# Performance work log

Measured on AMD Instinct MI355X. Metric: run time of the kernel, lower is better.

## Reference

```python
import jax, jax.numpy as jnp
import numpy as np

# ---- constants corresponding to undefined globals in the source repo ----
LN2 = float(np.log(2.0))
SIGMA2 = 1.0
W_F_COM, W_F_CRB = 1.0, 0.5
W_W_COM, W_W_CRB = 1.0, 0.5
BETA, EPS, ETA_F, ETA_W = 0.9, 1e-8, 0.01, 0.01


def _H(x):
    return jnp.conj(jnp.swapaxes(x, -1, -2))


def project_unit_modulus(F, eps=1e-12):
    mag = jnp.abs(F)
    safe = jnp.where(mag > eps, mag, 1.0).astype(F.dtype)
    return jnp.where(mag > eps, F / safe, jnp.zeros((), F.dtype))


def _power(F, W):
    # trace(F W W^H F^H) per (A,B) batch element, real
    FW = F @ W
    return jnp.sum(jnp.abs(FW) ** 2, axis=(-2, -1))


def normalize_power(F, W, Pt):
    s = jnp.sqrt(Pt / _power(F, W))
    return F * s[..., None, None].astype(F.dtype)


def normalize(F, W, Pt):
    s = jnp.sqrt(Pt / _power(F, W))
    return F, W * s[..., None, None].astype(W.dtype)


def grad_F_com(H, F, W):
    # H:[A,B,M,N]  F:[A,B,N,R]  W:[A,B,R,M]
    K_d = W.shape[0]
    V = W @ _H(W)                                   # [A,B,R,R]
    w_cols = jnp.swapaxes(W, -1, -2)[..., None]     # [A,B,M,R,1]
    V_mk = V[:, :, None] - w_cols @ _H(w_cols)      # [A,B,M,R,R]
    h = H[..., None]                                # [A,B,M,N,1]
    hHF = _H(h) @ F[:, :, None]                     # [A,B,M,1,R] = h^H F
    qf1 = (hHF @ V[:, :, None] @ _H(hHF))[..., 0, 0]   # h^H F V F^H h
    qf2 = (hHF @ V_mk @ _H(hHF))[..., 0, 0]
    d1 = LN2 * (qf1 + SIGMA2) + 1e-4
    d2 = LN2 * (qf2 + SIGMA2) + 1e-4
    HtF = h @ hHF                                   # [A,B,M,N,R] = (h h^H) F
    g1 = (HtF @ V[:, :, None]) / d1[..., None, None]
    g2 = (HtF @ V_mk) / d2[..., None, None]
    return (g1 - g2).sum(axis=2) / K_d


def _crb_core(F, W, A_dot, R_N_inv):
    Mm = _H(A_dot) @ R_N_inv @ A_dot                # [N,N]
    FHMF = _H(F) @ Mm @ F                           # [A,B,R,R]
    inner = _H(W) @ FHMF @ W                        # [A,B,M,M]
    tr = jnp.trace(inner, axis1=-2, axis2=-1)       # [A,B]
    return Mm, FHMF, tr


def grad_F_crb(F, W, A_dot, R_N_inv):
    Mm, _, tr = _crb_core(F, W, A_dot, R_N_inv)
    num = Mm @ F @ (W @ _H(W))                      # [A,B,N,R]
    return num / tr.reshape(1, -1, 1, 1)


def grad_W_crb(F, W, A_dot, R_N_inv):
    _, FHMF, tr = _crb_core(F, W, A_dot, R_N_inv)
    return (FHMF @ W) / tr.reshape(1, -1, 1, 1)


def grad_W_com(H, F, W):
    # Vectorised form of the per-antenna/user loop. In the original,
    # grad_W_1 == grad_W_2, so grad1 - masked(grad2) keeps only column m of term m.
    Mu = W.shape[-1]
    V = W @ _H(W)
    FHh = _H(F)[:, :, None] @ H[..., None]          # [A,B,M,R,1]
    Hbar = FHh @ _H(FHh)                            # [A,B,M,R,R] = F^H h h^H F
    tr = jnp.einsum('abij,abmji->abm', V, Hbar)     # trace(W W^H Hbar_m)
    denom = LN2 * (tr + SIGMA2)
    G = (Hbar @ W[:, :, None]) / denom[..., None, None]   # [A,B,M,R,M]
    return jnp.einsum('abmim->abim', G) / Mu


def get_sum_rate(H, F, W):
    G = jnp.abs(jnp.conj(H) @ F @ W) ** 2           # [A,B,M,M], (m,k)=|h_m^H F w_k|^2
    sig = jnp.diagonal(G, axis1=-2, axis2=-1)
    interf = G.sum(-1) - sig
    return jnp.log2(1.0 + sig / (interf + SIGMA2)).sum(-1)[0]   # [B]


def get_crb_fe(F, W, xi_0, A_dot, R_N_inv):
    _, _, tr = _crb_core(F, W, A_dot, R_N_inv)
    return (1.0 / (2.0 * xi_0 ** 2 * jnp.real(tr) + 1e-12))[0]  # [B]


def run_pga(H, F, W, xi_0, A_dot, R_N_inv, Pt, n_outer, n_inner, track=True):
    F = project_unit_modulus(F)
    F, W = normalize(F, W, Pt)
    B = H.shape[1]
    rates = jnp.zeros((n_outer, n_inner + 1, B), jnp.float32)
    crbs = jnp.zeros((n_outer, n_inner + 1, B), jnp.float32)
    s_F = jnp.zeros_like(F)
    s_W = jnp.zeros_like(W)
    for ii in range(n_outer):
        for jj in range(n_inner):
            gF = grad_F_com(H, F, W) * W_F_COM + grad_F_crb(F, W, A_dot, R_N_inv) * W_F_CRB
            s_F = BETA * s_F + (1.0 - BETA) * gF
            F = F + ETA_F * gF / (jnp.sqrt(s_F) + EPS)
            F = normalize_power(F, W, Pt)
            if track:
                rates = rates.at[ii, jj + 1].set(jax.lax.stop_gradient(get_sum_rate(H, F, W)))
                crbs = crbs.at[ii, jj + 1].set(jax.lax.stop_gradient(get_crb_fe(F, W, xi_0, A_dot, R_N_inv)))
        F = project_unit_modulus(F)
        gW0 = grad_W_com(H, F, W)[0] * W_W_COM + grad_W_crb(F, W, A_dot, R_N_inv)[0] * W_W_CRB
        s_W = s_W.at[0].set(BETA * s_W[0] + (1.0 - BETA) * gW0)
        W = W.at[0].set(W[0] + ETA_W * gW0 / (jnp.sqrt(s_W[0]) + EPS))
        F, W = normalize(F, W, Pt)
        if track:
            rates = rates.at[ii, 0].set(jax.lax.stop_gradient(get_sum_rate(H, F, W)))
            crbs = crbs.at[ii, 0].set(jax.lax.stop_gradient(get_crb_fe(F, W, xi_0, A_dot, R_N_inv)))
    rates = rates.reshape(n_outer * (n_inner + 1), B).T
    crbs = crbs.reshape(n_outer * (n_inner + 1), B).T
    return rates, crbs, F, W


def setup_inputs() -> dict:
    key = jax.random.key(0)
    ks = jax.random.split(key, 12)
    A, B, Mu, N, R, L = 1, 1024, 8, 64, 16, 64
    f32 = jnp.float32
    inp = dict(
        H_re=jax.random.normal(ks[0], (A, B, Mu, N), f32),
        H_im=jax.random.normal(ks[1], (A, B, Mu, N), f32),
        F0_re=jax.random.normal(ks[2], (A, B, N, R), f32),
        F0_im=jax.random.normal(ks[3], (A, B, N, R), f32),
        W0_re=jax.random.normal(ks[4], (A, B, R, Mu), f32),
        W0_im=jax.random.normal(ks[5], (A, B, R, Mu), f32),
        A_dot_re=jax.random.normal(ks[6], (L, N), f32),
        A_dot_im=jax.random.normal(ks[7], (L, N), f32),
    )
    # Build a PSD noise-covariance inverse so CRB trace denominators are well-conditioned.
    C = (jax.random.normal(ks[8], (L, L), f32) + 1j * jax.random.normal(ks[9], (L, L), f32)).astype(jnp.complex64)
    Rinv = (C @ jnp.conj(C.T)) / L + jnp.eye(L, dtype=jnp.complex64)
    inp['R_N_inv_re'] = jnp.real(Rinv)
    inp['R_N_inv_im'] = jnp.imag(Rinv)
    inp['xi_0'] = jnp.ones((1,), f32)
    inp['Pt'] = 10
    inp['n_iter_outer'] = 5
    inp['n_iter_inner'] = 4
    return inp


def reference(H_re, H_im, F0_re, F0_im, W0_re, W0_im, A_dot_re, A_dot_im,
              R_N_inv_re, R_N_inv_im, xi_0, Pt, n_iter_outer, n_iter_inner):
    c64 = jnp.complex64
    H = (H_re + 1j * H_im).astype(c64)
    F = (F0_re + 1j * F0_im).astype(c64)
    W = (W0_re + 1j * W0_im).astype(c64)
    A_dot = (A_dot_re + 1j * A_dot_im).astype(c64)
    R_N_inv = (R_N_inv_re + 1j * R_N_inv_im).astype(c64)
    return run_pga(H, F, W, xi_0, A_dot, R_N_inv, float(Pt), int(n_iter_outer), int(n_iter_inner), track=True)
```

## Files before the change

### kernel.cpp

```cpp
#include <hip/hip_runtime.h>
#include <math.h>

typedef float2 cf;

__device__ __forceinline__ cf mkc(float x, float y){ return make_float2(x,y); }
__device__ __forceinline__ cf lo4(float4 v){ return mkc(v.x, v.y); }
__device__ __forceinline__ cf hi4(float4 v){ return mkc(v.z, v.w); }


__device__ __forceinline__ void cmad(cf& acc, cf a, cf b){
    asm("v_pk_fma_f32 %0, %1, %2, %0 op_sel:[1,1,0] op_sel_hi:[1,0,1] neg_lo:[0,1,0]\n\t"
        "v_pk_fma_f32 %0, %1, %2, %0 op_sel:[0,0,0] op_sel_hi:[0,1,1]"
        : "+v"(acc) : "v"(a), "v"(b));
}
__device__ __forceinline__ void cmadc(cf& acc, cf a, cf b){
    asm("v_pk_fma_f32 %0, %1, %2, %0 op_sel:[1,1,0] op_sel_hi:[1,0,1] neg_hi:[0,1,0]\n\t"
        "v_pk_fma_f32 %0, %1, %2, %0 op_sel:[0,0,0] op_sel_hi:[0,1,1]"
        : "+v"(acc) : "v"(a), "v"(b));
}
__device__ __forceinline__ void cmad_bc(cf& acc, cf a, cf b){
    asm("v_pk_fma_f32 %0, %1, %2, %0 op_sel:[1,1,0] op_sel_hi:[0,1,1] neg_hi:[0,1,0]\n\t"
        "v_pk_fma_f32 %0, %1, %2, %0 op_sel:[0,0,0] op_sel_hi:[1,0,1]"
        : "+v"(acc) : "v"(a), "v"(b));
}
__device__ __forceinline__ void cmad_cc(cf& acc, cf a, cf b){
    asm("v_pk_fma_f32 %0, %1, %2, %0 op_sel:[1,1,0] op_sel_hi:[1,0,1] neg_lo:[0,1,0] neg_hi:[0,1,0]\n\t"
        "v_pk_fma_f32 %0, %1, %2, %0 op_sel:[0,0,0] op_sel_hi:[0,1,1] neg_hi:[0,1,0]"
        : "+v"(acc) : "v"(a), "v"(b));
}
__device__ __forceinline__ cf csqrtf2(cf z){
    float x = z.x, y = z.y;
    float r = hypotf(x, y);
    if (r == 0.0f) return mkc(0.f, 0.f);
    if (x >= 0.0f){
        float t = sqrtf(0.5f*(r + x));
        return mkc(t, 0.5f*y/t);
    } else {
        float t = sqrtf(0.5f*(r - x));
        return mkc(0.5f*fabsf(y)/t, copysignf(t, y));
    }
}
__device__ __forceinline__ cf cdiv(cf a, cf b){
    float inv = 1.0f/(b.x*b.x + b.y*b.y);
    return mkc((a.x*b.x + a.y*b.y)*inv, (a.y*b.x - a.x*b.y)*inv);
}

#define LN2F  0.69314718055994530942f
#define BETA_ 0.9f
#define OMB_  0.1f
#define EPS_  1e-8f
#define ETAF_ 0.01f
#define ETAW_ 0.01f

#define MM_S 66
#define F_S  18
#define FT_S 66
#define H_S  66
#define U_S  18
#define V_S  18

__device__ cf g_Mm[4096];

__device__ __forceinline__ float readScalarF(const int* p){
    int iv = *p;
    if (iv >= 0 && iv < 1000000) return (float)iv;
    return __int_as_float(iv);
}
__device__ __forceinline__ int readScalarI(const int* p){
    int iv = *p;
    if (iv >= 0 && iv < 1000000) return iv;
    return (int)(__int_as_float(iv) + 0.5f);
}

__device__ __forceinline__ float blockReduceSum(float v, float* slot, int tid){
    #pragma unroll
    for (int o = 32; o > 0; o >>= 1) v += __shfl_down(v, o, 64);
    if ((tid & 63) == 0) slot[tid >> 6] = v;
    __syncthreads();
    return slot[0] + slot[1] + slot[2] + slot[3];
}
__device__ __forceinline__ float2 blockReduceSum2(float a, float b2, float* sA, float* sB, int tid){
    #pragma unroll
    for (int o = 32; o > 0; o >>= 1){ a += __shfl_down(a, o, 64); b2 += __shfl_down(b2, o, 64); }
    if ((tid & 63) == 0){ sA[tid >> 6] = a; sB[tid >> 6] = b2; }
    __syncthreads();
    return make_float2(sA[0]+sA[1]+sA[2]+sA[3], sB[0]+sB[1]+sB[2]+sB[3]);
}

__device__ __forceinline__ void computeMF_T(const cf* sMm, const cf* sFT, cf* sMF, int tid){
    int j = tid & 15, nb = tid >> 4;
    cf a0=mkc(0,0), a1=mkc(0,0), a2=mkc(0,0), a3=mkc(0,0);
    const float4* ftrow = (const float4*)(sFT + j*FT_S);
    #pragma unroll
    for (int kkb = 0; kkb < 4; kkb++){
        cf f[16];
        #pragma unroll
        for (int q = 0; q < 8; q++){
            float4 v = ftrow[kkb*8+q];
            f[2*q] = lo4(v); f[2*q+1] = hi4(v);
        }
        const float4* m0 = (const float4*)(sMm + (nb    )*MM_S + kkb*16);
        const float4* m1 = (const float4*)(sMm + (nb+16 )*MM_S + kkb*16);
        const float4* m2 = (const float4*)(sMm + (nb+32 )*MM_S + kkb*16);
        const float4* m3 = (const float4*)(sMm + (nb+48 )*MM_S + kkb*16);
        #pragma unroll
        for (int q = 0; q < 8; q++){
            float4 v0 = m0[q], v1 = m1[q], v2 = m2[q], v3 = m3[q];
            cmad(a0, lo4(v0), f[2*q]); cmad(a0, hi4(v0), f[2*q+1]);
            cmad(a1, lo4(v1), f[2*q]); cmad(a1, hi4(v1), f[2*q+1]);
            cmad(a2, lo4(v2), f[2*q]); cmad(a2, hi4(v2), f[2*q+1]);
            cmad(a3, lo4(v3), f[2*q]); cmad(a3, hi4(v3), f[2*q+1]);
        }
    }
    sMF[(nb   )*F_S+j]=a0; sMF[(nb+16)*F_S+j]=a1;
    sMF[(nb+32)*F_S+j]=a2; sMF[(nb+48)*F_S+j]=a3;
}

__device__ __forceinline__ void uRefresh(const cf* sH, const cf* sFT, cf* sU, int tid){
    int h = tid & 1, j = (tid >> 1) & 15, m = tid >> 5;
    const float4* hp = (const float4*)(sH  + m*H_S);
    const float4* fp = (const float4*)(sFT + j*FT_S);
    cf acc = mkc(0,0);
    #pragma unroll
    for (int q = 0; q < 16; q++){
        int c = 2*q + h;
        float4 hv = hp[c], fv = fp[c];
        cmadc(acc, lo4(hv), lo4(fv));
        cmadc(acc, hi4(hv), hi4(fv));
    }
    acc.x += __shfl_xor(acc.x, 1, 64);
    acc.y += __shfl_xor(acc.y, 1, 64);
    if (h == 0) sU[m*U_S+j] = acc;
}

__device__ __forceinline__ float fwPartialOnly(const cf* sF, const cf* sW, int tid){
    int k = tid & 7, nb = tid >> 3;
    cf wcol[16];
    #pragma unroll
    for (int r = 0; r < 16; r++) wcol[r] = sW[r*8+k];
    float part = 0.f;
    #pragma unroll
    for (int rep = 0; rep < 2; rep++){
        int n = nb + rep*32;
        const float4* fr = (const float4*)(sF + n*F_S);
        cf acc = mkc(0,0);
        #pragma unroll
        for (int q = 0; q < 8; q++){
            float4 v = fr[q];
            cmad(acc, lo4(v), wcol[2*q]); cmad(acc, hi4(v), wcol[2*q+1]);
        }
        part += acc.x*acc.x + acc.y*acc.y;
    }
    return part;
}

__device__ __forceinline__ float2 fwTrcPartial(const cf* sF, const cf* sMF, const cf* sW, int tid){
    int k = tid & 7, nb = tid >> 3;
    cf wcol[16];
    #pragma unroll
    for (int r = 0; r < 16; r++) wcol[r] = sW[r*8+k];
    float part = 0.f, ptrc = 0.f;
    #pragma unroll
    for (int rep = 0; rep < 2; rep++){
        int n = nb + rep*32;
        const float4* fr = (const float4*)(sF + n*F_S);
        const float4* mr = (const float4*)(sMF + n*F_S);
        cf acc = mkc(0,0), acm = mkc(0,0);
        #pragma unroll
        for (int q = 0; q < 8; q++){
            float4 v = fr[q], m = mr[q];
            cmad(acc, lo4(v), wcol[2*q]); cmad(acc, hi4(v), wcol[2*q+1]);
            cmad(acm, lo4(m), wcol[2*q]); cmad(acm, hi4(m), wcol[2*q+1]);
        }
        part += acc.x*acc.x + acc.y*acc.y;
        ptrc += acc.x*acm.x + acc.y*acm.y;
    }
    return make_float2(part, ptrc);
}

__device__ __forceinline__ void ratesWave3(const cf* sU, const cf* sW, float mul,
                                           float* sRateVal, int tid){
    if (tid < 192) return;
    int l = tid - 192, m = l >> 3, k = l & 7;
    cf acc = mkc(0,0);
    #pragma unroll
    for (int j = 0; j < 16; j++) cmad(acc, sU[m*U_S+j], sW[j*8+k]);
    float p = acc.x*acc.x + acc.y*acc.y;
    float tot = p;
    #pragma unroll
    for (int mask = 4; mask >= 1; mask >>= 1) tot += __shfl_xor(tot, mask, 8);
    float sig = __shfl(p, 9*m, 64);
    float rate = log2f(1.0f + (mul*sig)/fmaf(mul, tot - sig, 1.0f));
    float val = (k == 0) ? rate : 0.0f;
    #pragma unroll
    for (int mask = 32; mask >= 1; mask >>= 1) val += __shfl_xor(val, mask, 64);
    if (l == 0) *sRateVal = val;
}

__global__ __launch_bounds__(256) void pga_prep(
    const float* __restrict__ Ar, const float* __restrict__ Ai,
    const float* __restrict__ Rr, const float* __restrict__ Ri)
{
    __shared__ cf sA[4096];
    __shared__ cf Tc[512];
    int tid = threadIdx.x;
    for (int idx = tid; idx < 4096; idx += 256)
        sA[idx] = mkc(Ar[idx], Ai[idx]);
    __syncthreads();
    for (int jb = 0; jb < 8; jb++){
        int j0 = jb*8;
        #pragma unroll
        for (int rep = 0; rep < 2; rep++){
            int idx = tid + rep*256;
            int p = idx >> 3, jc = idx & 7;
            cf acc = mkc(0,0);
            for (int q = 0; q < 64; q++){
                cf rv = mkc(Rr[p*64+q], Ri[p*64+q]);
                cmad(acc, rv, sA[q*64 + j0 + jc]);
            }
            Tc[idx] = acc;
        }
        __syncthreads();
        #pragma unroll
        for (int rep = 0; rep < 2; rep++){
            int idx = tid + rep*256;
            int i = idx >> 3, jc = idx & 7;
            cf acc = mkc(0,0);
            for (int p = 0; p < 64; p++)
                cmadc(acc, sA[p*64+i], Tc[p*8+jc]);
            g_Mm[i*64 + j0 + jc] = acc;
        }
        __syncthreads();
    }
}

__global__ __launch_bounds__(256) void pga_main(
    const float* __restrict__ Hre, const float* __restrict__ Him,
    const float* __restrict__ F0re, const float* __restrict__ F0im,
    const float* __restrict__ W0re, const float* __restrict__ W0im,
    const float* __restrict__ xi0p,
    const int* __restrict__ Ptp, const int* __restrict__ noutp, const int* __restrict__ ninnp,
    float* __restrict__ out, int B, int cplx)
{
    const int tid = threadIdx.x;
    const int b = blockIdx.x;

    __shared__ __align__(16) char sPool[72640];
    __shared__ float sRed[12];
    __shared__ float sRateVal;

    cf* sMm   = (cf*)(sPool + 0);
    cf* sF    = (cf*)(sPool + 33792);
    cf* sMF   = (cf*)(sPool + 43008);
    cf* sFT   = (cf*)(sPool + 52224);
    cf* sH    = (cf*)(sPool + 60672);
    cf* sW    = (cf*)(sPool + 64896);
    cf* sV    = (cf*)(sPool + 65920);
    cf* sU    = (cf*)(sPool + 68224);
    cf* sRow  = (cf*)(sPool + 69376);
    cf* sFHMF = (cf*)(sPool + 70400);
    cf* sCoefC= (cf*)(sPool + 72576);

    const float Pt    = readScalarF(Ptp);
    const int n_outer = readScalarI(noutp);
    const int n_inner = readScalarI(ninnp);
    const float xi0   = xi0p[0];
    const int nt = n_outer * (n_inner + 1);
    const float cxi = 2.0f*xi0*xi0;

    float* outR = out;
    float* outC = out + (size_t)B * nt;
    float* outF = out + (size_t)2 * B * nt;
    float* outW = outF + (cplx ? (size_t)B * 2048 : (size_t)B * 1024);

    cf fsf[4]; cf ssw = mkc(0.f, 0.f);
    {
        for (int idx = tid; idx < 4096; idx += 256){
            int r = idx >> 6, c = idx & 63;
            sMm[r*MM_S+c] = g_Mm[idx];
        }
        const float* hr = Hre + (size_t)b*512;
        const float* hi = Him + (size_t)b*512;
        for (int idx = tid; idx < 512; idx += 256){
            int m = idx >> 6, n = idx & 63;
            sH[m*H_S+n] = mkc(hr[idx], hi[idx]);
        }
        const float* fr = F0re + (size_t)b*1024;
        const float* fi = F0im + (size_t)b*1024;
        for (int idx = tid; idx < 1024; idx += 256){
            int n = idx >> 4, r = idx & 15;
            float re = fr[idx], im = fi[idx];
            float mag = hypotf(re, im);
            cf f = (mag > 1e-12f) ? mkc(re/mag, im/mag) : mkc(0.f, 0.f);
            sF[n*F_S+r] = f;
            sFT[r*FT_S+n] = f;
        }
        if (tid < 128)
            sW[tid] = mkc(W0re[(size_t)b*128 + tid], W0im[(size_t)b*128 + tid]);
        #pragma unroll
        for (int rep = 0; rep < 4; rep++) fsf[rep] = mkc(0.f, 0.f);
    }
    __syncthreads();

    uRefresh(sH, sFT, sU, tid);
    {
        float pw0 = blockReduceSum(fwPartialOnly(sF, sW, tid), sRed+0, tid);
        float s0 = sqrtf(Pt / pw0);
        if (tid < 128){ cf w = sW[tid]; sW[tid] = mkc(w.x*s0, w.y*s0); }
    }
    computeMF_T(sMm, sFT, sMF, tid);
    __syncthreads();

    float sp = 1.0f, sp2 = 1.0f;

    for (int ii = 0; ii < n_outer; ii++){
        {
            int i = tid >> 4, jx = tid & 15;
            cf acc = mkc(0,0);
            #pragma unroll
            for (int k = 0; k < 8; k++) cmad_bc(acc, sW[i*8+k], sW[jx*8+k]);
            sV[i*V_S+jx] = acc;
        }
        __syncthreads();

        for (int jj = 0; jj < n_inner; jj++){
            const int j = tid & 15, nb = tid >> 4;

            cf vrow[16];
            {
                const float4* vp = (const float4*)(sV + j*V_S);
                #pragma unroll
                for (int q = 0; q < 8; q++){
                    float4 v = vp[q];
                    vrow[2*q] = lo4(v); vrow[2*q+1] = hi4(v);
                }
            }
            float ptr_ = 0.f;
            cf G[4];
            #pragma unroll
            for (int rep = 0; rep < 4; rep++){
                int n = nb + rep*16;
                const float4* mr = (const float4*)(sMF + n*F_S);
                cf acc = mkc(0,0);
                #pragma unroll
                for (int q = 0; q < 8; q++){
                    float4 v = mr[q];
                    cmad_bc(acc, lo4(v), vrow[2*q]); cmad_bc(acc, hi4(v), vrow[2*q+1]);
                }
                G[rep] = acc;
                cf f = sF[n*F_S+j];
                ptr_ += f.x*acc.x + f.y*acc.y;
            }
            if (tid < 128){
                int m = tid >> 4;
                const float4* up = (const float4*)(sU + m*U_S);
                cf t2 = mkc(0,0);
                #pragma unroll
                for (int q = 0; q < 8; q++){
                    float4 uv = up[q];
                    cmad_bc(t2, lo4(uv), vrow[2*q]); cmad_bc(t2, hi4(uv), vrow[2*q+1]);
                }
                cf u = sU[m*U_S+j];
                float qv = t2.x*u.x + t2.y*u.y;
                cf c = mkc(0,0); cmad(c, u, sW[j*8+m]);
                #pragma unroll
                for (int mask = 8; mask >= 1; mask >>= 1){
                    qv  += __shfl_xor(qv,  mask, 16);
                    c.x += __shfl_xor(c.x, mask, 16);
                    c.y += __shfl_xor(c.y, mask, 16);
                }
                float cc = c.x*c.x + c.y*c.y;
                float inv1 = 1.0f/(LN2F*(sp2*qv + 1.0f) + 1e-4f);
                float inv2 = 1.0f/(LN2F*(sp2*(qv - cc) + 1.0f) + 1e-4f);
                float a = inv1 - inv2;
                cf ci = mkc(c.x*inv2, c.y*inv2);
                cf row = mkc(t2.x*a, t2.y*a);
                cmad_bc(row, ci, sW[j*8+m]);
                sRow[tid] = row;
            }
            if (jj > 0) ratesWave3(sU, sW, sp2, &sRateVal, tid);
            float tr = blockReduceSum(ptr_, sRed+0, tid);
            if (jj > 0 && tid == 0){
                int t = ii*(n_inner+1) + jj;
                size_t base = (size_t)b*nt;
                outR[base + t] = sRateVal;
                outC[base + t] = 1.0f/(cxi*(sp2*tr) + 1e-12f);
            }

            {
                float hinv = 0.5f/(sp*tr);
                cf rowj[8];
                #pragma unroll
                for (int m = 0; m < 8; m++){
                    cf r = sRow[m*16+j];
                    rowj[m] = mkc(sp*r.x, sp*r.y);
                }
                #pragma unroll
                for (int rep = 0; rep < 4; rep++){
                    int n = nb + rep*16;
                    cf g = mkc(G[rep].x*hinv, G[rep].y*hinv);
                    #pragma unroll
                    for (int m = 0; m < 8; m++) cmad(g, sH[m*H_S+n], rowj[m]);
                    cf sf = fsf[rep];
                    sf.x = BETA_*sf.x + OMB_*g.x;
                    sf.y = BETA_*sf.y + OMB_*g.y;
                    fsf[rep] = sf;
                    cf d = csqrtf2(sf); d.x += EPS_;
                    cf upd = cdiv(g, d);
                    cf f = sF[n*F_S+j];
                    cf fn = mkc(fmaf(ETAF_, upd.x, sp*f.x), fmaf(ETAF_, upd.y, sp*f.y));
                    sF[n*F_S+j] = fn;
                    sFT[j*FT_S+n] = fn;
                }
            }
            __syncthreads();

            computeMF_T(sMm, sFT, sMF, tid);
            float part = fwPartialOnly(sF, sW, tid);
            uRefresh(sH, sFT, sU, tid);
            float pw = blockReduceSum(part, sRed+4, tid);
            float s = sqrtf(Pt / pw);
            sp = s; sp2 = s*s;

            if (jj == n_inner-1){
                cf vrow2[16];
                {
                    const float4* vp2 = (const float4*)(sV + j*V_S);
                    #pragma unroll
                    for (int q = 0; q < 8; q++){
                        float4 v = vp2[q];
                        vrow2[2*q] = lo4(v); vrow2[2*q+1] = hi4(v);
                    }
                }
                float ptrl = 0.f;
                #pragma unroll
                for (int rep = 0; rep < 4; rep++){
                    int n = nb + rep*16;
                    const float4* mr = (const float4*)(sMF + n*F_S);
                    cf acc = mkc(0,0);
                    #pragma unroll
                    for (int q = 0; q < 8; q++){
                        float4 v = mr[q];
                        cmad_bc(acc, lo4(v), vrow2[2*q]); cmad_bc(acc, hi4(v), vrow2[2*q+1]);
                    }
                    cf f = sF[n*F_S+j];
                    ptrl += f.x*acc.x + f.y*acc.y;
                }
                ratesWave3(sU, sW, sp2, &sRateVal, tid);
                float trl = blockReduceSum(ptrl, sRed+8, tid);
                if (tid == 0){
                    int t = ii*(n_inner+1) + n_inner;
                    size_t base = (size_t)b*nt;
                    outR[base + t] = sRateVal;
                    outC[base + t] = 1.0f/(cxi*(sp2*trl) + 1e-12f);
                }
            }
        }

        const int j = tid & 15, nb = tid >> 4;
        {
            #pragma unroll
            for (int rep = 0; rep < 4; rep++){
                int n = nb + rep*16;
                cf f = sF[n*F_S+j];
                float mag = hypotf(f.x, f.y);
                cf fp = (sp*mag > 1e-12f) ? mkc(f.x/mag, f.y/mag) : mkc(0.f, 0.f);
                sF[n*F_S+j] = fp;
                sFT[j*FT_S+n] = fp;
            }
            sp = 1.0f; sp2 = 1.0f;
        }
        __syncthreads();
        computeMF_T(sMm, sFT, sMF, tid);
        uRefresh(sH, sFT, sU, tid);
        __syncthreads();
        float ptr2;
        {
            int i = tid >> 4;
            const float4* fti = (const float4*)(sFT + i*FT_S);
            cf acc = mkc(0,0);
            #pragma unroll
            for (int q = 0; q < 32; q++){
                float4 fv = fti[q];
                cmadc(acc, lo4(fv), sMF[(2*q  )*F_S+j]);
                cmadc(acc, hi4(fv), sMF[(2*q+1)*F_S+j]);
            }
            sFHMF[i*17+j] = acc;
            cf v = sV[j*V_S+i];
            ptr2 = acc.x*v.x - acc.y*v.y;
        }
        if (tid < 128){
            int m = tid >> 4, r = tid & 15;
            cf u_mr = sU[m*U_S+r];
            const float4* up = (const float4*)(sU + m*U_S);
            cf t2 = mkc(0,0);
            #pragma unroll
            for (int q = 0; q < 8; q++){
                float4 uv = up[q];
                cmad_cc(t2, sV[(2*q)*V_S+r],   lo4(uv));
                cmad_cc(t2, sV[(2*q+1)*V_S+r], hi4(uv));
            }
            float trm = u_mr.x*t2.x - u_mr.y*t2.y;
            cf a = mkc(0,0); cmad(a, u_mr, sW[r*8+m]);
            #pragma unroll
            for (int mask = 8; mask >= 1; mask >>= 1){
                trm += __shfl_xor(trm, mask, 16);
                a.x += __shfl_xor(a.x, mask, 16);
                a.y += __shfl_xor(a.y, mask, 16);
            }
            if (r == 0){
                float invd = 1.0f/(LN2F*(trm + 1.0f)*8.0f);
                sCoefC[m] = mkc(a.x*invd, a.y*invd);
            }
        }
        float trW = blockReduceSum(ptr2, sRed+0, tid);
        cf gw = mkc(0,0);
        if (tid < 128){
            int i2 = tid >> 3, mm = tid & 7;
            cf acc = mkc(0,0);
            #pragma unroll
            for (int j2 = 0; j2 < 16; j2++) cmad(acc, sFHMF[i2*17+j2], sW[j2*8+mm]);
            float hinv = 0.5f / trW;
            gw = mkc(acc.x*hinv, acc.y*hinv);
            cmadc(gw, sU[mm*U_S+i2], sCoefC[mm]);
        }
        __syncthreads();
        if (tid < 128){
            cf sw = ssw;
            sw.x = BETA_*sw.x + OMB_*gw.x;
            sw.y = BETA_*sw.y + OMB_*gw.y;
            ssw = sw;
            cf d = csqrtf2(sw); d.x += EPS_;
            cf upd = cdiv(gw, d);
            cf w = sW[tid];
            w.x = fmaf(ETAW_, upd.x, w.x);
            w.y = fmaf(ETAW_, upd.y, w.y);
            sW[tid] = w;
        }
        __syncthreads();
        float2 pq = fwTrcPartial(sF, sMF, sW, tid);
        float2 pr = blockReduceSum2(pq.x, pq.y, sRed+4, sRed+8, tid);
        float s2 = sqrtf(Pt / pr.x);
        float s2sq = s2*s2;
        ratesWave3(sU, sW, s2sq, &sRateVal, tid);
        __syncthreads();
        if (tid < 128){
            cf w = sW[tid];
            sW[tid] = mkc(w.x*s2, w.y*s2);
        }
        if (tid == 0){
            int t = ii*(n_inner+1);
            size_t base = (size_t)b*nt;
            outR[base + t] = sRateVal;
            outC[base + t] = 1.0f/(cxi*(s2sq*pr.y) + 1e-12f);
        }
        __syncthreads();
    }

    if (cplx){
        int j = tid & 15, nb = tid >> 4;
        #pragma unroll
        for (int rep = 0; rep < 4; rep++){
            int n = nb + rep*16;
            cf f = sF[n*F_S+j];
            size_t o = ((size_t)b*1024 + (size_t)(tid + rep*256))*2;
            outF[o]   = f.x;
            outF[o+1] = f.y;
        }
        if (tid < 128){
            cf w = sW[tid];
            size_t o = ((size_t)b*128 + tid)*2;
            outW[o]   = w.x;
            outW[o+1] = w.y;
        }
    } else {
        int j = tid & 15, nb = tid >> 4;
        #pragma unroll
        for (int rep = 0; rep < 4; rep++){
            int n = nb + rep*16;
            outF[(size_t)b*1024 + (size_t)(tid + rep*256)] = sF[n*F_S+j].x;
        }
        if (tid < 128)
            outW[(size_t)b*128 + tid] = sW[tid].x;
    }
}

extern "C" void kernel_launch(void* const* d_in, const int* in_sizes, int n_in,
                              void* d_out, int out_size, void* d_ws, size_t ws_size,
                              hipStream_t stream)
{
    (void)n_in; (void)d_ws; (void)ws_size;
    int B = in_sizes[0] / 512;

    long S = (long)out_size;
    long numI = S - 2304L*B;
    long numR = S - 1152L*B;
    bool okI = (numI > 0) && (numI % (2L*B) == 0) && (numI/(2L*B) >= 1) && (numI/(2L*B) <= 256);
    bool okR = (numR > 0) && (numR % (2L*B) == 0) && (numR/(2L*B) >= 1) && (numR/(2L*B) <= 256);
    int cplx = okI ? 1 : (okR ? 0 : 1);

    pga_prep<<<1, 256, 0, stream>>>(
        (const float*)d_in[6], (const float*)d_in[7],
        (const float*)d_in[8], (const float*)d_in[9]);

    pga_main<<<B, 256, 0, stream>>>(
        (const float*)d_in[0], (const float*)d_in[1],
        (const float*)d_in[2], (const float*)d_in[3],
        (const float*)d_in[4], (const float*)d_in[5],
        (const float*)d_in[10],
        (const int*)d_in[11], (const int*)d_in[12], (const int*)d_in[13],
        (float*)d_out, B, cplx);
}
```

Baseline: 663.0 us.

## Double block size to 512 threads and halve per-thread work in PGA main kernel

Launches pga_main with 512 threads per block instead of 256 and redistributes per-thread loops (MF product, power partials, gradient rows, output stores) so each thread handles half as many rows. Phases that only map to 256 threads are gated with tid<256, the rate computation moves to the last wave, and block reductions now sum eight wave slots. The aim is more latency hiding and shorter serial chains per block, at the cost of higher LDS-limited occupancy pressure, idle lanes in the gated phases, and more expensive barriers.

```diff
diff --git a/kernel.cpp b/kernel.cpp
--- a/kernel.cpp
+++ b/kernel.cpp
@@ -77,19 +77,21 @@
     for (int o = 32; o > 0; o >>= 1) v += __shfl_down(v, o, 64);
     if ((tid & 63) == 0) slot[tid >> 6] = v;
     __syncthreads();
-    return slot[0] + slot[1] + slot[2] + slot[3];
+    return ((slot[0]+slot[1])+(slot[2]+slot[3]))+((slot[4]+slot[5])+(slot[6]+slot[7]));
 }
 __device__ __forceinline__ float2 blockReduceSum2(float a, float b2, float* sA, float* sB, int tid){
     #pragma unroll
     for (int o = 32; o > 0; o >>= 1){ a += __shfl_down(a, o, 64); b2 += __shfl_down(b2, o, 64); }
     if ((tid & 63) == 0){ sA[tid >> 6] = a; sB[tid >> 6] = b2; }
     __syncthreads();
-    return make_float2(sA[0]+sA[1]+sA[2]+sA[3], sB[0]+sB[1]+sB[2]+sB[3]);
+    float ra = ((sA[0]+sA[1])+(sA[2]+sA[3]))+((sA[4]+sA[5])+(sA[6]+sA[7]));
+    float rb = ((sB[0]+sB[1])+(sB[2]+sB[3]))+((sB[4]+sB[5])+(sB[6]+sB[7]));
+    return make_float2(ra, rb);
 }
 
 __device__ __forceinline__ void computeMF_T(const cf* sMm, const cf* sFT, cf* sMF, int tid){
     int j = tid & 15, nb = tid >> 4;
-    cf a0=mkc(0,0), a1=mkc(0,0), a2=mkc(0,0), a3=mkc(0,0);
+    cf a0=mkc(0,0), a1=mkc(0,0);
     const float4* ftrow = (const float4*)(sFT + j*FT_S);
     #pragma unroll
     for (int kkb = 0; kkb < 4; kkb++){
@@ -100,20 +102,15 @@
             f[2*q] = lo4(v); f[2*q+1] = hi4(v);
         }
         const float4* m0 = (const float4*)(sMm + (nb    )*MM_S + kkb*16);
-        const float4* m1 = (const float4*)(sMm + (nb+16 )*MM_S + kkb*16);
-        const float4* m2 = (const float4*)(sMm + (nb+32 )*MM_S + kkb*16);
-        const float4* m3 = (const float4*)(sMm + (nb+48 )*MM_S + kkb*16);
+        const float4* m1 = (const float4*)(sMm + (nb+32 )*MM_S + kkb*16);
         #pragma unroll
         for (int q = 0; q < 8; q++){
-            float4 v0 = m0[q], v1 = m1[q], v2 = m2[q], v3 = m3[q];
+            float4 v0 = m0[q], v1 = m1[q];
             cmad(a0, lo4(v0), f[2*q]); cmad(a0, hi4(v0), f[2*q+1]);
             cmad(a1, lo4(v1), f[2*q]); cmad(a1, hi4(v1), f[2*q+1]);
-            cmad(a2, lo4(v2), f[2*q]); cmad(a2, hi4(v2), f[2*q+1]);
-            cmad(a3, lo4(v3), f[2*q]); cmad(a3, hi4(v3), f[2*q+1]);
-        }
-    }
-    sMF[(nb   )*F_S+j]=a0; sMF[(nb+16)*F_S+j]=a1;
-    sMF[(nb+32)*F_S+j]=a2; sMF[(nb+48)*F_S+j]=a3;
+        }
+    }
+    sMF[(nb   )*F_S+j]=a0; sMF[(nb+32)*F_S+j]=a1;
 }
 
 __device__ __forceinline__ void uRefresh(const cf* sH, const cf* sFT, cf* sU, int tid){
@@ -134,54 +131,43 @@
 }
 
 __device__ __forceinline__ float fwPartialOnly(const cf* sF, const cf* sW, int tid){
-    int k = tid & 7, nb = tid >> 3;
+    int k = tid & 7, n = tid >> 3;
     cf wcol[16];
     #pragma unroll
     for (int r = 0; r < 16; r++) wcol[r] = sW[r*8+k];
-    float part = 0.f;
-    #pragma unroll
-    for (int rep = 0; rep < 2; rep++){
-        int n = nb + rep*32;
-        const float4* fr = (const float4*)(sF + n*F_S);
-        cf acc = mkc(0,0);
-        #pragma unroll
-        for (int q = 0; q < 8; q++){
-            float4 v = fr[q];
-            cmad(acc, lo4(v), wcol[2*q]); cmad(acc, hi4(v), wcol[2*q+1]);
-        }
-        part += acc.x*acc.x + acc.y*acc.y;
-    }
-    return part;
+    const float4* fr = (const float4*)(sF + n*F_S);
+    cf acc = mkc(0,0);
+    #pragma unroll
+    for (int q = 0; q < 8; q++){
+        float4 v = fr[q];
+        cmad(acc, lo4(v), wcol[2*q]); cmad(acc, hi4(v), wcol[2*q+1]);
+    }
+    return acc.x*acc.x + acc.y*acc.y;
 }
 
 __device__ __forceinline__ float2 fwTrcPartial(const cf* sF, const cf* sMF, const cf* sW, int tid){
-    int k = tid & 7, nb = tid >> 3;
+    int k = tid & 7, n = tid >> 3;
     cf wcol[16];
     #pragma unroll
     for (int r = 0; r < 16; r++) wcol[r] = sW[r*8+k];
-    float part = 0.f, ptrc = 0.f;
-    #pragma unroll
-    for (int rep = 0; rep < 2; rep++){
-        int n = nb + rep*32;
-        const float4* fr = (const float4*)(sF + n*F_S);
-        const float4* mr = (const float4*)(sMF + n*F_S);
-        cf acc = mkc(0,0), acm = mkc(0,0);
-        #pragma unroll
-        for (int q = 0; q < 8; q++){
-            float4 v = fr[q], m = mr[q];
-            cmad(acc, lo4(v), wcol[2*q]); cmad(acc, hi4(v), wcol[2*q+1]);
-            cmad(acm, lo4(m), wcol[2*q]); cmad(acm, hi4(m), wcol[2*q+1]);
-        }
-        part += acc.x*acc.x + acc.y*acc.y;
-        ptrc += acc.x*acm.x + acc.y*acm.y;
-    }
+    const float4* fr = (const float4*)(sF + n*F_S);
+    const float4* mr = (const float4*)(sMF + n*F_S);
+    cf acc = mkc(0,0), acm = mkc(0,0);
+    #pragma unroll
+    for (int q = 0; q < 8; q++){
+        float4 v = fr[q], m = mr[q];
+        cmad(acc, lo4(v), wcol[2*q]); cmad(acc, hi4(v), wcol[2*q+1]);
+        cmad(acm, lo4(m), wcol[2*q]); cmad(acm, hi4(m), wcol[2*q+1]);
+    }
+    float part = acc.x*acc.x + acc.y*acc.y;
+    float ptrc = acc.x*acm.x + acc.y*acm.y;
     return make_float2(part, ptrc);
 }
 
-__device__ __forceinline__ void ratesWave3(const cf* sU, const cf* sW, float mul,
+__device__ __forceinline__ void ratesWave7(const cf* sU, const cf* sW, float mul,
                                            float* sRateVal, int tid){
-    if (tid < 192) return;
-    int l = tid - 192, m = l >> 3, k = l & 7;
+    if (tid < 448) return;
+    int l = tid - 448, m = l >> 3, k = l & 7;
     cf acc = mkc(0,0);
     #pragma unroll
     for (int j = 0; j < 16; j++) cmad(acc, sU[m*U_S+j], sW[j*8+k]);
@@ -234,7 +220,7 @@
     }
 }
 
-__global__ __launch_bounds__(256) void pga_main(
+__global__ __launch_bounds__(512) void pga_main(
     const float* __restrict__ Hre, const float* __restrict__ Him,
     const float* __restrict__ F0re, const float* __restrict__ F0im,
     const float* __restrict__ W0re, const float* __restrict__ W0im,
@@ -246,7 +232,7 @@
     const int b = blockIdx.x;
 
     __shared__ __align__(16) char sPool[72640];
-    __shared__ float sRed[12];
+    __shared__ float sRed[24];
     __shared__ float sRateVal;
 
     cf* sMm   = (cf*)(sPool + 0);
@@ -273,21 +259,21 @@
     float* outF = out + (size_t)2 * B * nt;
     float* outW = outF + (cplx ? (size_t)B * 2048 : (size_t)B * 1024);
 
-    cf fsf[4]; cf ssw = mkc(0.f, 0.f);
+    cf fsf[2]; cf ssw = mkc(0.f, 0.f);
     {
-        for (int idx = tid; idx < 4096; idx += 256){
+        for (int idx = tid; idx < 4096; idx += 512){
             int r = idx >> 6, c = idx & 63;
             sMm[r*MM_S+c] = g_Mm[idx];
         }
         const float* hr = Hre + (size_t)b*512;
         const float* hi = Him + (size_t)b*512;
-        for (int idx = tid; idx < 512; idx += 256){
-            int m = idx >> 6, n = idx & 63;
-            sH[m*H_S+n] = mkc(hr[idx], hi[idx]);
+        {
+            int m = tid >> 6, n = tid & 63;
+            sH[m*H_S+n] = mkc(hr[tid], hi[tid]);
         }
         const float* fr = F0re + (size_t)b*1024;
         const float* fi = F0im + (size_t)b*1024;
-        for (int idx = tid; idx < 1024; idx += 256){
+        for (int idx = tid; idx < 1024; idx += 512){
             int n = idx >> 4, r = idx & 15;
             float re = fr[idx], im = fi[idx];
             float mag = hypotf(re, im);
@@ -297,12 +283,11 @@
         }
         if (tid < 128)
             sW[tid] = mkc(W0re[(size_t)b*128 + tid], W0im[(size_t)b*128 + tid]);
-        #pragma unroll
-        for (int rep = 0; rep < 4; rep++) fsf[rep] = mkc(0.f, 0.f);
+        fsf[0] = mkc(0.f, 0.f); fsf[1] = mkc(0.f, 0.f);
     }
     __syncthreads();
 
-    uRefresh(sH, sFT, sU, tid);
+    if (tid < 256) uRefresh(sH, sFT, sU, tid);
     {
         float pw0 = blockReduceSum(fwPartialOnly(sF, sW, tid), sRed+0, tid);
         float s0 = sqrtf(Pt / pw0);
@@ -314,7 +299,7 @@
     float sp = 1.0f, sp2 = 1.0f;
 
     for (int ii = 0; ii < n_outer; ii++){
-        {
+        if (tid < 256){
             int i = tid >> 4, jx = tid & 15;
             cf acc = mkc(0,0);
             #pragma unroll
@@ -336,10 +321,10 @@
                 }
             }
             float ptr_ = 0.f;
-            cf G[4];
-            #pragma unroll
-            for (int rep = 0; rep < 4; rep++){
-                int n = nb + rep*16;
+            cf G[2];
+            #pragma unroll
+            for (int rep = 0; rep < 2; rep++){
+                int n = nb + rep*32;
                 const float4* mr = (const float4*)(sMF + n*F_S);
                 cf acc = mkc(0,0);
                 #pragma unroll
@@ -378,7 +363,7 @@
                 cmad_bc(row, ci, sW[j*8+m]);
                 sRow[tid] = row;
             }
-            if (jj > 0) ratesWave3(sU, sW, sp2, &sRateVal, tid);
+            if (jj > 0) ratesWave7(sU, sW, sp2, &sRateVal, tid);
             float tr = blockReduceSum(ptr_, sRed+0, tid);
             if (jj > 0 && tid == 0){
                 int t = ii*(n_inner+1) + jj;
@@ -396,8 +381,8 @@
                     rowj[m] = mkc(sp*r.x, sp*r.y);
                 }
                 #pragma unroll
-                for (int rep = 0; rep < 4; rep++){
-                    int n = nb + rep*16;
+                for (int rep = 0; rep < 2; rep++){
+                    int n = nb + rep*32;
                     cf g = mkc(G[rep].x*hinv, G[rep].y*hinv);
                     #pragma unroll
                     for (int m = 0; m < 8; m++) cmad(g, sH[m*H_S+n], rowj[m]);
@@ -417,8 +402,8 @@
 
             computeMF_T(sMm, sFT, sMF, tid);
             float part = fwPartialOnly(sF, sW, tid);
-            uRefresh(sH, sFT, sU, tid);
-            float pw = blockReduceSum(part, sRed+4, tid);
+            if (tid < 256) uRefresh(sH, sFT, sU, tid);
+            float pw = blockReduceSum(part, sRed+8, tid);
             float s = sqrtf(Pt / pw);
             sp = s; sp2 = s*s;
 
@@ -434,8 +419,8 @@
                 }
                 float ptrl = 0.f;
                 #pragma unroll
-                for (int rep = 0; rep < 4; rep++){
-                    int n = nb + rep*16;
+                for (int rep = 0; rep < 2; rep++){
+                    int n = nb + rep*32;
                     const float4* mr = (const float4*)(sMF + n*F_S);
                     cf acc = mkc(0,0);
                     #pragma unroll
@@ -446,8 +431,8 @@
                     cf f = sF[n*F_S+j];
                     ptrl += f.x*acc.x + f.y*acc.y;
                 }
-                ratesWave3(sU, sW, sp2, &sRateVal, tid);
-                float trl = blockReduceSum(ptrl, sRed+8, tid);
+                ratesWave7(sU, sW, sp2, &sRateVal, tid);
+                float trl = blockReduceSum(ptrl, sRed+16, tid);
                 if (tid == 0){
                     int t = ii*(n_inner+1) + n_inner;
                     size_t base = (size_t)b*nt;
@@ -460,8 +445,8 @@
         const int j = tid & 15, nb = tid >> 4;
         {
             #pragma unroll
-            for (int rep = 0; rep < 4; rep++){
-                int n = nb + rep*16;
+            for (int rep = 0; rep < 2; rep++){
+                int n = nb + rep*32;
                 cf f = sF[n*F_S+j];
                 float mag = hypotf(f.x, f.y);
                 cf fp = (sp*mag > 1e-12f) ? mkc(f.x/mag, f.y/mag) : mkc(0.f, 0.f);
@@ -472,10 +457,10 @@
         }
         __syncthreads();
         computeMF_T(sMm, sFT, sMF, tid);
-        uRefresh(sH, sFT, sU, tid);
-        __syncthreads();
-        float ptr2;
-        {
+        if (tid < 256) uRefresh(sH, sFT, sU, tid);
+        __syncthreads();
+        float ptr2 = 0.f;
+        if (tid < 256){
             int i = tid >> 4;
             const float4* fti = (const float4*)(sFT + i*FT_S);
             cf acc = mkc(0,0);
@@ -539,10 +524,10 @@
         }
         __syncthreads();
         float2 pq = fwTrcPartial(sF, sMF, sW, tid);
-        float2 pr = blockReduceSum2(pq.x, pq.y, sRed+4, sRed+8, tid);
+        float2 pr = blockReduceSum2(pq.x, pq.y, sRed+8, sRed+16, tid);
         float s2 = sqrtf(Pt / pr.x);
         float s2sq = s2*s2;
-        ratesWave3(sU, sW, s2sq, &sRateVal, tid);
+        ratesWave7(sU, sW, s2sq, &sRateVal, tid);
         __syncthreads();
         if (tid < 128){
             cf w = sW[tid];
@@ -560,10 +545,10 @@
     if (cplx){
         int j = tid & 15, nb = tid >> 4;
         #pragma unroll
-        for (int rep = 0; rep < 4; rep++){
-            int n = nb + rep*16;
+        for (int rep = 0; rep < 2; rep++){
+            int n = nb + rep*32;
             cf f = sF[n*F_S+j];
-            size_t o = ((size_t)b*1024 + (size_t)(tid + rep*256))*2;
+            size_t o = ((size_t)b*1024 + (size_t)(tid + rep*512))*2;
             outF[o]   = f.x;
             outF[o+1] = f.y;
         }
@@ -576,9 +561,9 @@
     } else {
         int j = tid & 15, nb = tid >> 4;
         #pragma unroll
-        for (int rep = 0; rep < 4; rep++){
-            int n = nb + rep*16;
-            outF[(size_t)b*1024 + (size_t)(tid + rep*256)] = sF[n*F_S+j].x;
+        for (int rep = 0; rep < 2; rep++){
+            int n = nb + rep*32;
+            outF[(size_t)b*1024 + (size_t)(tid + rep*512)] = sF[n*F_S+j].x;
         }
         if (tid < 128)
             outW[(size_t)b*128 + tid] = sW[tid].x;
@@ -603,7 +588,7 @@
         (const float*)d_in[6], (const float*)d_in[7],
         (const float*)d_in[8], (const float*)d_in[9]);
 
-    pga_main<<<B, 256, 0, stream>>>(
+    pga_main<<<B, 512, 0, stream>>>(
         (const float*)d_in[0], (const float*)d_in[1],
         (const float*)d_in[2], (const float*)d_in[3],
         (const float*)d_in[4], (const float*)d_in[5],
```

Result: slower. 861.1 us (+29.9%).
